# Performance work log

Measured on AMD Instinct MI355X. Metric: run time of the kernel, lower is better.

## Reference

```python
import jax, jax.numpy as jnp
import numpy as np
from jax import lax

BS, C, S = 2, 32, 64  # cubic volume: h == w == d required by the module's views
EPS = 1e-5


def setup_inputs() -> dict:
    key = jax.random.key(0)
    kq, kk, kv, kw, kb, kg = jax.random.split(key, 6)
    q = jax.random.normal(kq, (BS, C, S, S, S), dtype=jnp.float32)
    k = jax.random.normal(kk, (BS, C, S, S, S), dtype=jnp.float32)
    v = jax.random.normal(kv, (BS, C, S, S, S), dtype=jnp.float32)
    # Conv_3x3x3: Conv3d(3*C -> C, k=3, pad=1, bias) + BatchNorm3d(C) (eval) + ReLU
    fan_in = 3 * C * 27
    conv_w = jax.random.normal(kw, (C, 3 * C, 3, 3, 3), dtype=jnp.float32) / np.sqrt(fan_in)
    conv_b = jax.random.normal(kb, (C,), dtype=jnp.float32) * 0.01
    bn_gamma = jnp.ones((C,), jnp.float32)
    bn_beta = jnp.zeros((C,), jnp.float32)
    bn_mean = jnp.zeros((C,), jnp.float32)
    bn_var = jnp.ones((C,), jnp.float32)
    return {"q": q, "k": k, "v": v, "conv_w": conv_w, "conv_b": conv_b,
            "bn_gamma": bn_gamma, "bn_beta": bn_beta, "bn_mean": bn_mean, "bn_var": bn_var}


def _axial_attention(q, k, v):
    # q,k,v: (b, c, h, w, d) with h == w == d == S. All three per-slice python
    # loops of the original collapse into batched einsums (dropout is eval -> identity).
    # Branch a: per d-slice s, A[i,j] = softmax_j(sum_m q[b,c,m,i,s] k[b,c,m,j,s])
    A = jax.nn.softmax(jnp.einsum('bcmis,bcmjs->bcsij', q, k), axis=-1)
    AVa = jnp.einsum('bcsij,bcjws->bciws', A, v)          # (b,c,h,w,d)
    # Branch b: per w-slice s, attention over h with feature dim d
    A = jax.nn.softmax(jnp.einsum('bcism,bcjsm->bcsij', q, k), axis=-1)
    AVb = jnp.einsum('bcsij,bcjsm->bcism', A, v)          # (b,c,h,w,d)
    # Branch c: per h-slice s, attention over w with feature dim d
    A = jax.nn.softmax(jnp.einsum('bcsim,bcsjm->bcsij', q, k), axis=-1)
    AVc = jnp.einsum('bcsij,bcsjm->bcsim', A, v)          # (b,c,h,w,d)
    return jnp.concatenate([AVa, AVb, AVc], axis=1)       # (b,3c,h,w,d)


def reference(q, k, v, conv_w, conv_b, bn_gamma, bn_beta, bn_mean, bn_var):
    x = _axial_attention(q, k, v)
    x = lax.conv_general_dilated(x, conv_w, window_strides=(1, 1, 1), padding='SAME',
                                 dimension_numbers=('NCDHW', 'OIDHW', 'NCDHW'))
    x = x + conv_b[None, :, None, None, None]
    inv = bn_gamma / jnp.sqrt(bn_var + EPS)
    x = x * inv[None, :, None, None, None] + (bn_beta - bn_mean * inv)[None, :, None, None, None]
    return jax.nn.relu(x)
```

## Files before the change

kernel.cpp:

```cpp
#include <hip/hip_runtime.h>
#include <hip/hip_bf16.h>


#define CH 32

typedef __attribute__((ext_vector_type(8))) _Float16 f16x8;
typedef __attribute__((ext_vector_type(4))) _Float16 f16x4;
typedef __attribute__((ext_vector_type(8))) short bf16x8;
typedef __attribute__((ext_vector_type(4))) float f32x4;

static __device__ __forceinline__ unsigned short f2bf(float f) {
  union { float f; unsigned u; } x; x.f = f;
  unsigned r = x.u + 0x7fff + ((x.u >> 16) & 1);
  return (unsigned short)(r >> 16);
}

__global__ __launch_bounds__(256) void trans_dwh(const float* __restrict__ q,
                                                 const float* __restrict__ k,
                                                 const float* __restrict__ v,
                                                 _Float16* __restrict__ qT,
                                                 _Float16* __restrict__ kT,
                                                 _Float16* __restrict__ vT,
                                                 _Float16* __restrict__ qF,
                                                 _Float16* __restrict__ kF,
                                                 _Float16* __restrict__ vF,
                                                 int b) {
  __shared__ __align__(16) _Float16 Ls[64 * 72];
  const int blk = blockIdx.x;
  const int c = blk >> 6;
  const int w = blk & 63;
  const int tid = threadIdx.x;
  const size_t bc = (size_t)(b * CH + c);
  const float* srcs[3] = {q, k, v};
  _Float16* dsts[3] = {qT, kT, vT};
  _Float16* dstsF[3] = {qF, kF, vF};
  const int h = tid >> 2, dq = tid & 3;

  for (int tz = 0; tz < 3; ++tz) {
    const float* sp = srcs[tz] + bc * 262144 + (size_t)h * 4096 + (size_t)w * 64;
    float4 ld[4];
    #pragma unroll
    for (int pp = 0; pp < 4; ++pp) {
      const int d0 = dq * 16 + pp * 4;
      ld[pp] = *(const float4*)(sp + d0);
      Ls[(d0 + 0) * 72 + h] = (_Float16)ld[pp].x;
      Ls[(d0 + 1) * 72 + h] = (_Float16)ld[pp].y;
      Ls[(d0 + 2) * 72 + h] = (_Float16)ld[pp].z;
      Ls[(d0 + 3) * 72 + h] = (_Float16)ld[pp].w;
    }
    {
      _Float16* fp = dstsF[tz] + (size_t)c * 262144 + (size_t)h * 4096 +
                     (size_t)w * 64 + dq * 16;
      f16x8 lo8 = {(_Float16)ld[0].x, (_Float16)ld[0].y, (_Float16)ld[0].z, (_Float16)ld[0].w,
                   (_Float16)ld[1].x, (_Float16)ld[1].y, (_Float16)ld[1].z, (_Float16)ld[1].w};
      f16x8 hi8 = {(_Float16)ld[2].x, (_Float16)ld[2].y, (_Float16)ld[2].z, (_Float16)ld[2].w,
                   (_Float16)ld[3].x, (_Float16)ld[3].y, (_Float16)ld[3].z, (_Float16)ld[3].w};
      *(f16x8*)(fp) = lo8;
      *(f16x8*)(fp + 8) = hi8;
    }
    __syncthreads();
    _Float16* dp = dsts[tz] + (size_t)c * 262144 + (size_t)w * 64;
    #pragma unroll
    for (int p = 0; p < 2; ++p) {
      const int idx = p * 256 + tid;
      const int d = idx >> 3, o = (idx & 7) * 8;
      *(f16x8*)(dp + (size_t)d * 4096 + o) = *(const f16x8*)&Ls[d * 72 + o];
    }
    __syncthreads();
  }
}

__device__ __forceinline__ void attn_core(_Float16 (&Qh)[64][72],
                                          _Float16 (&Kh)[64][72],
                                          _Float16 (&Vh)[64][72],
                                          bool v_transposed,
                                          unsigned short* __restrict__ ydst,
                                          int c, int s, int tid) {
  const int w = tid >> 6;
  const int lane = tid & 63;
  const int r = lane & 15;
  const int oct = lane >> 4;

  f32x4 sc[4];
  #pragma unroll
  for (int jt = 0; jt < 4; ++jt) sc[jt] = (f32x4){0.f, 0.f, 0.f, 0.f};
  f16x8 aq0 = *(const f16x8*)&Qh[w * 16 + r][oct * 8];
  f16x8 aq1 = *(const f16x8*)&Qh[w * 16 + r][32 + oct * 8];
  #pragma unroll
  for (int jt = 0; jt < 4; ++jt) {
    f16x8 bk0 = *(const f16x8*)&Kh[jt * 16 + r][oct * 8];
    f16x8 bk1 = *(const f16x8*)&Kh[jt * 16 + r][32 + oct * 8];
    sc[jt] = __builtin_amdgcn_mfma_f32_16x16x32_f16(aq0, bk0, sc[jt], 0, 0, 0);
    sc[jt] = __builtin_amdgcn_mfma_f32_16x16x32_f16(aq1, bk1, sc[jt], 0, 0, 0);
  }

  float P[4][4];
  #pragma unroll
  for (int reg = 0; reg < 4; ++reg) {
    float mx = fmaxf(fmaxf(sc[0][reg], sc[1][reg]), fmaxf(sc[2][reg], sc[3][reg]));
    mx = fmaxf(mx, __shfl_xor(mx, 1));
    mx = fmaxf(mx, __shfl_xor(mx, 2));
    mx = fmaxf(mx, __shfl_xor(mx, 4));
    mx = fmaxf(mx, __shfl_xor(mx, 8));
    float e[4], sum = 0.f;
    #pragma unroll
    for (int jt = 0; jt < 4; ++jt) { e[jt] = __expf(sc[jt][reg] - mx); sum += e[jt]; }
    sum += __shfl_xor(sum, 1);
    sum += __shfl_xor(sum, 2);
    sum += __shfl_xor(sum, 4);
    sum += __shfl_xor(sum, 8);
    const float inv = 1.f / sum;
    #pragma unroll
    for (int jt = 0; jt < 4; ++jt) P[reg][jt] = e[jt] * inv;
  }

  #pragma unroll
  for (int reg = 0; reg < 4; ++reg)
    #pragma unroll
    for (int jt = 0; jt < 4; ++jt)
      Qh[w * 16 + oct * 4 + reg][jt * 16 + r] = (_Float16)P[reg][jt];

  f16x8 ap0 = *(const f16x8*)&Qh[w * 16 + r][oct * 8];
  f16x8 ap1 = *(const f16x8*)&Qh[w * 16 + r][32 + oct * 8];
  f32x4 ot[4];
  #pragma unroll
  for (int tt = 0; tt < 4; ++tt) {
    ot[tt] = (f32x4){0.f, 0.f, 0.f, 0.f};
    f16x8 bv0, bv1;
    if (v_transposed) {
      bv0 = *(const f16x8*)&Vh[tt * 16 + r][oct * 8];
      bv1 = *(const f16x8*)&Vh[tt * 16 + r][32 + oct * 8];
    } else {
      #pragma unroll
      for (int e = 0; e < 8; ++e) {
        bv0[e] = Vh[oct * 8 + e][tt * 16 + r];
        bv1[e] = Vh[32 + oct * 8 + e][tt * 16 + r];
      }
    }
    ot[tt] = __builtin_amdgcn_mfma_f32_16x16x32_f16(ap0, bv0, ot[tt], 0, 0, 0);
    ot[tt] = __builtin_amdgcn_mfma_f32_16x16x32_f16(ap1, bv1, ot[tt], 0, 0, 0);
  }

  __syncthreads();
  unsigned short* Ot = (unsigned short*)&Kh[0][0];
  #pragma unroll
  for (int tt = 0; tt < 4; ++tt)
    #pragma unroll
    for (int reg = 0; reg < 4; ++reg)
      Ot[(size_t)(w * 16 + oct * 4 + reg) * 72 + tt * 16 + r] = f2bf(ot[tt][reg]);
  __syncthreads();

  {
    const int i = tid >> 2, seg = tid & 3;
    const unsigned short* src = Ot + (size_t)i * 72 + seg * 16;
    bf16x8 a0 = *(const bf16x8*)(src);
    bf16x8 a1 = *(const bf16x8*)(src + 8);
    unsigned short* dst = ydst + ((size_t)(c * 64 + s)) * 4096 + tid * 16;
    *(bf16x8*)(dst) = a0;
    *(bf16x8*)(dst + 8) = a1;
  }
}

__global__ __launch_bounds__(256) void attn0(const _Float16* __restrict__ qT,
                                             const _Float16* __restrict__ kT,
                                             const _Float16* __restrict__ vT,
                                             unsigned short* __restrict__ y0b) {
  __shared__ __align__(16) _Float16 Qh[64][72];
  __shared__ __align__(16) _Float16 Kh[64][72];
  __shared__ __align__(16) _Float16 Vh[64][72];

  const int blk0 = blockIdx.x;
  const int blk = ((blk0 & 7) << 8) | (blk0 >> 3);
  const int s = blk & 63;
  const int c = blk >> 6;
  const int tid = threadIdx.x;

  const _Float16* qp = qT + ((size_t)c * 64 + s) * 4096;
  const _Float16* kp = kT + ((size_t)c * 64 + s) * 4096;
  const _Float16* vp = vT + ((size_t)c * 64 + s) * 4096;
  #pragma unroll
  for (int ii = 0; ii < 2; ++ii) {
    const int idx = ii * 256 + tid;
    const int row = idx >> 3, ch = (idx & 7) * 8;
    *(f16x8*)&Qh[row][ch] = *(const f16x8*)(qp + row * 64 + ch);
    *(f16x8*)&Kh[row][ch] = *(const f16x8*)(kp + row * 64 + ch);
    *(f16x8*)&Vh[row][ch] = *(const f16x8*)(vp + row * 64 + ch);
  }
  __syncthreads();
  attn_core(Qh, Kh, Vh, true, y0b, c, s, tid);
}

__global__ __launch_bounds__(256) void attn12(const _Float16* __restrict__ qF,
                                              const _Float16* __restrict__ kF,
                                              const _Float16* __restrict__ vF,
                                              unsigned short* __restrict__ y1b,
                                              unsigned short* __restrict__ y2b) {
  __shared__ __align__(16) _Float16 Qh[64][72];
  __shared__ __align__(16) _Float16 Kh[64][72];
  __shared__ __align__(16) _Float16 Vh[64][72];

  const int blk0 = blockIdx.x;
  const int blk = ((blk0 & 7) << 9) | (blk0 >> 3);
  const int br2 = blk >> 11;
  const int inner = blk & 2047;
  const int s = inner & 63;
  const int c = inner >> 6;
  const int tid = threadIdx.x;

  const size_t base = (size_t)c * 262144;
  #pragma unroll
  for (int ii = 0; ii < 2; ++ii) {
    const int idx = ii * 256 + tid;
    const int row = idx >> 3, ch = (idx & 7) * 8;
    const size_t off = br2 ? ((size_t)s * 4096 + (size_t)row * 64 + ch)
                           : ((size_t)row * 4096 + (size_t)s * 64 + ch);
    *(f16x8*)&Qh[row][ch] = *(const f16x8*)(qF + base + off);
    *(f16x8*)&Kh[row][ch] = *(const f16x8*)(kF + base + off);
    *(f16x8*)&Vh[row][ch] = *(const f16x8*)(vF + base + off);
  }
  __syncthreads();
  attn_core(Qh, Kh, Vh, false, br2 ? y2b : y1b, c, s, tid);
}

__global__ __launch_bounds__(256) void repack_all(const unsigned short* __restrict__ y0p,
                                                  const unsigned short* __restrict__ y1p,
                                                  const unsigned short* __restrict__ y2p,
                                                  unsigned short* __restrict__ xblk,
                                                  int b) {
  __shared__ unsigned short Ls[32 * 530];
  const int blk = blockIdx.x;
  const int br = blk >> 9;
  const int inner = blk & 511;
  const int oc = inner & 7;
  const int z = inner >> 3;
  const int tid = threadIdx.x;
  const int c = tid & 31;
  const int w8 = tid >> 5;

  const unsigned short* ybr = (br == 0) ? y0p : (br == 1) ? y1p : y2p;

  size_t src;
  if (br == 2) src = ((size_t)(c * 64 + z)) * 4096 + (size_t)(oc * 8 + w8) * 64;
  else         src = ((size_t)(c * 64 + oc * 8 + w8)) * 4096 + (size_t)z * 64;

  #pragma unroll
  for (int kk = 0; kk < 8; ++kk) {
    bf16x8 vv = *(const bf16x8*)(ybr + src + kk * 8);
    #pragma unroll
    for (int e = 0; e < 8; ++e) {
      const int l = kk * 8 + e;
      const int li = (br == 0) ? (l * 8 + w8) : (w8 * 64 + l);
      Ls[c * 530 + li] = (unsigned short)vv[e];
    }
  }
  __syncthreads();

  unsigned short* xq = xblk + ((size_t)(b * 3 + br)) * 262144 * 32;
  #pragma unroll
  for (int p = 0; p < 2; ++p) {
    const int o = p * 256 + tid;
    bf16x8 o0, o1, o2, o3;
    #pragma unroll
    for (int e = 0; e < 8; ++e) {
      o0[e] = (short)Ls[(e)      * 530 + o];
      o1[e] = (short)Ls[(8 + e)  * 530 + o];
      o2[e] = (short)Ls[(16 + e) * 530 + o];
      o3[e] = (short)Ls[(24 + e) * 530 + o];
    }
    int sp;
    if (br == 0) sp = z * 4096 + (o >> 3) * 64 + oc * 8 + (o & 7);
    else         sp = z * 4096 + oc * 512 + o;
    unsigned short* dst = xq + (size_t)sp * 32;
    *(bf16x8*)(dst)      = o0;
    *(bf16x8*)(dst + 8)  = o1;
    *(bf16x8*)(dst + 16) = o2;
    *(bf16x8*)(dst + 24) = o3;
  }
}

__global__ __launch_bounds__(256) void wprep(const float* __restrict__ w,
                                             unsigned short* __restrict__ wt2) {
  int idx = blockIdx.x * 256 + threadIdx.x;
  if (idx >= 27 * 32 * 96) return;
  int tap = idx / 3072;
  int rem = idx - tap * 3072;
  int co = rem / 96, ci = rem - co * 96;
  int ciq = ci >> 5, oct = (ci >> 3) & 3, e = ci & 7;
  wt2[(((tap * 3 + ciq) * 4 + oct) * 32 + co) * 8 + e] =
      f2bf(w[((size_t)co * 96 + ci) * 27 + tap]);
}

__global__ __launch_bounds__(256, 2) void conv_mfma(const unsigned short* __restrict__ xblk,
                                                    const unsigned short* __restrict__ wt2,
                                                    const float* __restrict__ cb,
                                                    const float* __restrict__ gamma,
                                                    const float* __restrict__ beta,
                                                    const float* __restrict__ mean,
                                                    const float* __restrict__ var,
                                                    float* __restrict__ out) {
  __shared__ __align__(16) unsigned short XT[23760];

  const int blk0 = blockIdx.x;
  const int blk = ((blk0 & 7) << 6) | (blk0 >> 3);
  const int yt = blk & 7;
  const int zp = (blk >> 3) & 31;
  const int b = blk >> 8;
  const int tid = threadIdx.x;
  const int w = tid >> 6;
  const int lane = tid & 63;
  const int r = lane & 15;
  const int oct = lane >> 4;
  const int y0 = yt * 8;
  const int z0 = zp * 2;

  f32x4 acc0[2][4][2], acc1[2][4][2];
  #pragma unroll
  for (int ry = 0; ry < 2; ++ry)
    #pragma unroll
    for (int xc = 0; xc < 4; ++xc)
      #pragma unroll
      for (int ct = 0; ct < 2; ++ct) {
        acc0[ry][xc][ct] = (f32x4){0.f, 0.f, 0.f, 0.f};
        acc1[ry][xc][ct] = (f32x4){0.f, 0.f, 0.f, 0.f};
      }

  auto STAGE = [&](int p, int ciq) {
    const unsigned short* xq = xblk + ((size_t)(b * 3 + ciq)) * (262144ull * 32) +
                               (size_t)p * (4096 * 32);
    #pragma unroll
    for (int ii = 0; ii < 11; ++ii) {
      const int idx = ii * 256 + tid;
      if (idx < 2640) {
        const int row = idx / 264;
        const int rem = idx - row * 264;
        const int x = rem >> 2;
        const int cq = rem & 3;
        const int gy = y0 + row - 1, gx = x - 1;
        bf16x8 val = {0, 0, 0, 0, 0, 0, 0, 0};
        if ((unsigned)gy < 64u && (unsigned)gx < 64u)
          val = *(const bf16x8*)(xq + (size_t)(gy * 64 + gx) * 32 + cq * 8);
        *(bf16x8*)&XT[row * 2376 + x * 36 + cq * 8] = val;
      }
    }
  };

  auto C2 = [&](int dzA, int dzB, int ciq) {
    #pragma unroll
    for (int dy = 0; dy < 3; ++dy) {
      #pragma unroll
      for (int dx = 0; dx < 3; ++dx) {
        const unsigned short* wpA =
            wt2 + ((size_t)((((dzA * 3 + dy) * 3 + dx) * 3 + ciq) * 4 + oct)) * 256;
        const unsigned short* wpB =
            wt2 + ((size_t)((((dzB * 3 + dy) * 3 + dx) * 3 + ciq) * 4 + oct)) * 256;
        bf16x8 wA0 = *(const bf16x8*)(wpA + r * 8);
        bf16x8 wA1 = *(const bf16x8*)(wpA + 128 + r * 8);
        bf16x8 wB0 = *(const bf16x8*)(wpB + r * 8);
        bf16x8 wB1 = *(const bf16x8*)(wpB + 128 + r * 8);
        #pragma unroll
        for (int ry = 0; ry < 2; ++ry) {
          const int lrow = w * 2 + ry + dy;
          #pragma unroll
          for (int xc = 0; xc < 4; ++xc) {
            bf16x8 af = *(const bf16x8*)&XT[lrow * 2376 + (xc * 16 + r + dx) * 36 + oct * 8];
            acc0[ry][xc][0] = __builtin_amdgcn_mfma_f32_16x16x32_bf16(af, wA0, acc0[ry][xc][0], 0, 0, 0);
            acc0[ry][xc][1] = __builtin_amdgcn_mfma_f32_16x16x32_bf16(af, wA1, acc0[ry][xc][1], 0, 0, 0);
            acc1[ry][xc][0] = __builtin_amdgcn_mfma_f32_16x16x32_bf16(af, wB0, acc1[ry][xc][0], 0, 0, 0);
            acc1[ry][xc][1] = __builtin_amdgcn_mfma_f32_16x16x32_bf16(af, wB1, acc1[ry][xc][1], 0, 0, 0);
          }
        }
      }
    }
  };

  auto C1 = [&](f32x4 (&A)[2][4][2], int dz, int ciq) {
    #pragma unroll
    for (int dy = 0; dy < 3; ++dy) {
      #pragma unroll
      for (int dx = 0; dx < 3; ++dx) {
        const unsigned short* wp =
            wt2 + ((size_t)((((dz * 3 + dy) * 3 + dx) * 3 + ciq) * 4 + oct)) * 256;
        bf16x8 w0 = *(const bf16x8*)(wp + r * 8);
        bf16x8 w1 = *(const bf16x8*)(wp + 128 + r * 8);
        #pragma unroll
        for (int ry = 0; ry < 2; ++ry) {
          const int lrow = w * 2 + ry + dy;
          #pragma unroll
          for (int xc = 0; xc < 4; ++xc) {
            bf16x8 af = *(const bf16x8*)&XT[lrow * 2376 + (xc * 16 + r + dx) * 36 + oct * 8];
            A[ry][xc][0] = __builtin_amdgcn_mfma_f32_16x16x32_bf16(af, w0, A[ry][xc][0], 0, 0, 0);
            A[ry][xc][1] = __builtin_amdgcn_mfma_f32_16x16x32_bf16(af, w1, A[ry][xc][1], 0, 0, 0);
          }
        }
      }
    }
  };

  #pragma unroll
  for (int ps = 0; ps < 4; ++ps) {
    const int p = z0 - 1 + ps;
    if ((unsigned)p > 63u) continue;
    for (int ciq = 0; ciq < 3; ++ciq) {
      __syncthreads();
      STAGE(p, ciq);
      __syncthreads();
      if (ps == 0)      C1(acc0, 0, ciq);
      else if (ps == 3) C1(acc1, 2, ciq);
      else              C2(ps, ps - 1, ciq);
    }
  }

  float invc[2], shc[2], bic[2];
  #pragma unroll
  for (int ct = 0; ct < 2; ++ct) {
    const int co = ct * 16 + r;
    const float iv = gamma[co] * rsqrtf(var[co] + 1e-5f);
    invc[ct] = iv;
    shc[ct] = beta[co] - mean[co] * iv;
    bic[ct] = cb[co];
  }

  auto STO = [&](f32x4 (&A)[2][4][2], int z) {
    #pragma unroll
    for (int ct = 0; ct < 2; ++ct) {
      float* oc = out + (((size_t)(b * CH + ct * 16 + r)) << 18) + ((size_t)z << 12);
      #pragma unroll
      for (int ry = 0; ry < 2; ++ry) {
        const int y = y0 + w * 2 + ry;
        #pragma unroll
        for (int xc = 0; xc < 4; ++xc) {
          const f32x4 a = A[ry][xc][ct];
          float4 st;
          st.x = fmaxf(0.f, (a[0] + bic[ct]) * invc[ct] + shc[ct]);
          st.y = fmaxf(0.f, (a[1] + bic[ct]) * invc[ct] + shc[ct]);
          st.z = fmaxf(0.f, (a[2] + bic[ct]) * invc[ct] + shc[ct]);
          st.w = fmaxf(0.f, (a[3] + bic[ct]) * invc[ct] + shc[ct]);
          *(float4*)(oc + (size_t)y * 64 + xc * 16 + oct * 4) = st;
        }
      }
    }
  };
  STO(acc0, z0);
  STO(acc1, z0 + 1);
}

extern "C" void kernel_launch(void* const* d_in, const int* in_sizes, int n_in,
                              void* d_out, int out_size, void* d_ws, size_t ws_size,
                              hipStream_t stream) {
  const float* q     = (const float*)d_in[0];
  const float* k     = (const float*)d_in[1];
  const float* v     = (const float*)d_in[2];
  const float* cw    = (const float*)d_in[3];
  const float* cb    = (const float*)d_in[4];
  const float* gamma = (const float*)d_in[5];
  const float* beta  = (const float*)d_in[6];
  const float* mean  = (const float*)d_in[7];
  const float* var   = (const float*)d_in[8];

  unsigned short* xblk = (unsigned short*)d_ws;
  unsigned short* y0b  = (unsigned short*)((char*)d_ws + (96ull  << 20));
  _Float16*       qT   = (_Float16*)((char*)d_ws + (112ull << 20));
  _Float16*       kT   = (_Float16*)((char*)d_ws + (128ull << 20));
  _Float16*       vT   = (_Float16*)((char*)d_ws + (144ull << 20));
  unsigned short* wt2  = (unsigned short*)((char*)d_ws + (160ull << 20));
  _Float16* qF = (_Float16*)((char*)d_ws + (48ull << 20));
  _Float16* kF = (_Float16*)((char*)d_ws + (64ull << 20));
  _Float16* vF = (_Float16*)((char*)d_ws + (80ull << 20));
  unsigned short* y1b = (unsigned short*)kT;
  unsigned short* y2b = (unsigned short*)vT;
  float* out = (float*)d_out;

  hipLaunchKernelGGL(wprep, dim3(324), dim3(256), 0, stream, cw, wt2);
  for (int b = 0; b < 2; ++b) {
    hipLaunchKernelGGL(trans_dwh, dim3(2048), dim3(256), 0, stream,
                       q, k, v, qT, kT, vT, qF, kF, vF, b);
    hipLaunchKernelGGL(attn0, dim3(2048), dim3(256), 0, stream, qT, kT, vT, y0b);
    hipLaunchKernelGGL(attn12, dim3(4096), dim3(256), 0, stream,
                       qF, kF, vF, y1b, y2b);
    hipLaunchKernelGGL(repack_all, dim3(1536), dim3(256), 0, stream,
                       y0b, y1b, y2b, xblk, b);
  }
  hipLaunchKernelGGL(conv_mfma, dim3(512), dim3(256), 0, stream,
                     xblk, wt2, cb, gamma, beta, mean, var, out);
}
```

Before: 333.5 us.

## Switch conv to 32x32x16 bf16 MFMA with weights as A operand

The 3D conv kernel moves from 16x16x32 MFMA tiles to 32x32x16 tiles, with the weights as the A operand (32 output channels) and 32 x-positions as B. The weight prep is re-laid out per lane to match the new operand format. Each tile now reuses more operands per instruction, so fewer LDS reads and weight loads are issued per FLOP. The cost is that the epilogue now writes scalar floats per channel register rather than float4 vectors, and per-channel BN constants are recomputed inside the store loop.

```diff
diff --git a/kernel.cpp b/kernel.cpp
--- a/kernel.cpp
+++ b/kernel.cpp
@@ -8,6 +8,7 @@
 typedef __attribute__((ext_vector_type(4))) _Float16 f16x4;
 typedef __attribute__((ext_vector_type(8))) short bf16x8;
 typedef __attribute__((ext_vector_type(4))) float f32x4;
+typedef __attribute__((ext_vector_type(16))) float f32x16;
 
 static __device__ __forceinline__ unsigned short f2bf(float f) {
   union { float f; unsigned u; } x; x.f = f;
@@ -279,19 +280,20 @@
 }
 
 __global__ __launch_bounds__(256) void wprep(const float* __restrict__ w,
-                                             unsigned short* __restrict__ wt2) {
+                                             unsigned short* __restrict__ wt3) {
   int idx = blockIdx.x * 256 + threadIdx.x;
-  if (idx >= 27 * 32 * 96) return;
-  int tap = idx / 3072;
-  int rem = idx - tap * 3072;
-  int co = rem / 96, ci = rem - co * 96;
-  int ciq = ci >> 5, oct = (ci >> 3) & 3, e = ci & 7;
-  wt2[(((tap * 3 + ciq) * 4 + oct) * 32 + co) * 8 + e] =
-      f2bf(w[((size_t)co * 96 + ci) * 27 + tap]);
+  if (idx >= 27 * 6 * 64 * 8) return;
+  const int e = idx & 7;
+  const int lane = (idx >> 3) & 63;
+  const int rest = idx >> 9;
+  const int tap = rest / 6, ksg = rest - tap * 6;
+  const int co = lane & 31, kg = lane >> 5;
+  const int ci = ksg * 16 + kg * 8 + e;
+  wt3[idx] = f2bf(w[((size_t)co * 96 + ci) * 27 + tap]);
 }
 
 __global__ __launch_bounds__(256, 2) void conv_mfma(const unsigned short* __restrict__ xblk,
-                                                    const unsigned short* __restrict__ wt2,
+                                                    const unsigned short* __restrict__ wt3,
                                                     const float* __restrict__ cb,
                                                     const float* __restrict__ gamma,
                                                     const float* __restrict__ beta,
@@ -308,20 +310,20 @@
   const int tid = threadIdx.x;
   const int w = tid >> 6;
   const int lane = tid & 63;
-  const int r = lane & 15;
-  const int oct = lane >> 4;
+  const int x32 = lane & 31;
+  const int kg = lane >> 5;
   const int y0 = yt * 8;
   const int z0 = zp * 2;
 
-  f32x4 acc0[2][4][2], acc1[2][4][2];
+  f32x16 acc0[2][2], acc1[2][2];
   #pragma unroll
   for (int ry = 0; ry < 2; ++ry)
     #pragma unroll
-    for (int xc = 0; xc < 4; ++xc)
+    for (int xc = 0; xc < 2; ++xc)
       #pragma unroll
-      for (int ct = 0; ct < 2; ++ct) {
-        acc0[ry][xc][ct] = (f32x4){0.f, 0.f, 0.f, 0.f};
-        acc1[ry][xc][ct] = (f32x4){0.f, 0.f, 0.f, 0.f};
+      for (int e = 0; e < 16; ++e) {
+        acc0[ry][xc][e] = 0.f;
+        acc1[ry][xc][e] = 0.f;
       }
 
   auto STAGE = [&](int p, int ciq) {
@@ -346,50 +348,52 @@
 
   auto C2 = [&](int dzA, int dzB, int ciq) {
     #pragma unroll
-    for (int dy = 0; dy < 3; ++dy) {
+    for (int ks = 0; ks < 2; ++ks) {
       #pragma unroll
-      for (int dx = 0; dx < 3; ++dx) {
-        const unsigned short* wpA =
-            wt2 + ((size_t)((((dzA * 3 + dy) * 3 + dx) * 3 + ciq) * 4 + oct)) * 256;
-        const unsigned short* wpB =
-            wt2 + ((size_t)((((dzB * 3 + dy) * 3 + dx) * 3 + ciq) * 4 + oct)) * 256;
-        bf16x8 wA0 = *(const bf16x8*)(wpA + r * 8);
-        bf16x8 wA1 = *(const bf16x8*)(wpA + 128 + r * 8);
-        bf16x8 wB0 = *(const bf16x8*)(wpB + r * 8);
-        bf16x8 wB1 = *(const bf16x8*)(wpB + 128 + r * 8);
+      for (int dy = 0; dy < 3; ++dy) {
         #pragma unroll
-        for (int ry = 0; ry < 2; ++ry) {
-          const int lrow = w * 2 + ry + dy;
+        for (int dx = 0; dx < 3; ++dx) {
+          const unsigned short* wpA =
+              wt3 + ((size_t)(((dzA * 3 + dy) * 3 + dx) * 6 + ciq * 2 + ks) * 64 + lane) * 8;
+          const unsigned short* wpB =
+              wt3 + ((size_t)(((dzB * 3 + dy) * 3 + dx) * 6 + ciq * 2 + ks) * 64 + lane) * 8;
+          bf16x8 wA = *(const bf16x8*)wpA;
+          bf16x8 wB = *(const bf16x8*)wpB;
           #pragma unroll
-          for (int xc = 0; xc < 4; ++xc) {
-            bf16x8 af = *(const bf16x8*)&XT[lrow * 2376 + (xc * 16 + r + dx) * 36 + oct * 8];
-            acc0[ry][xc][0] = __builtin_amdgcn_mfma_f32_16x16x32_bf16(af, wA0, acc0[ry][xc][0], 0, 0, 0);
-            acc0[ry][xc][1] = __builtin_amdgcn_mfma_f32_16x16x32_bf16(af, wA1, acc0[ry][xc][1], 0, 0, 0);
-            acc1[ry][xc][0] = __builtin_amdgcn_mfma_f32_16x16x32_bf16(af, wB0, acc1[ry][xc][0], 0, 0, 0);
-            acc1[ry][xc][1] = __builtin_amdgcn_mfma_f32_16x16x32_bf16(af, wB1, acc1[ry][xc][1], 0, 0, 0);
+          for (int ry = 0; ry < 2; ++ry) {
+            const int lrow = w * 2 + ry + dy;
+            #pragma unroll
+            for (int xc = 0; xc < 2; ++xc) {
+              bf16x8 af = *(const bf16x8*)&XT[lrow * 2376 + (xc * 32 + x32 + dx) * 36 +
+                                              (ks * 2 + kg) * 8];
+              acc0[ry][xc] = __builtin_amdgcn_mfma_f32_32x32x16_bf16(wA, af, acc0[ry][xc], 0, 0, 0);
+              acc1[ry][xc] = __builtin_amdgcn_mfma_f32_32x32x16_bf16(wB, af, acc1[ry][xc], 0, 0, 0);
+            }
           }
         }
       }
     }
   };
 
-  auto C1 = [&](f32x4 (&A)[2][4][2], int dz, int ciq) {
-    #pragma unroll
-    for (int dy = 0; dy < 3; ++dy) {
+  auto C1 = [&](f32x16 (&A)[2][2], int dz, int ciq) {
+    #pragma unroll
+    for (int ks = 0; ks < 2; ++ks) {
       #pragma unroll
-      for (int dx = 0; dx < 3; ++dx) {
-        const unsigned short* wp =
-            wt2 + ((size_t)((((dz * 3 + dy) * 3 + dx) * 3 + ciq) * 4 + oct)) * 256;
-        bf16x8 w0 = *(const bf16x8*)(wp + r * 8);
-        bf16x8 w1 = *(const bf16x8*)(wp + 128 + r * 8);
+      for (int dy = 0; dy < 3; ++dy) {
         #pragma unroll
-        for (int ry = 0; ry < 2; ++ry) {
-          const int lrow = w * 2 + ry + dy;
+        for (int dx = 0; dx < 3; ++dx) {
+          const unsigned short* wp =
+              wt3 + ((size_t)(((dz * 3 + dy) * 3 + dx) * 6 + ciq * 2 + ks) * 64 + lane) * 8;
+          bf16x8 wf = *(const bf16x8*)wp;
           #pragma unroll
-          for (int xc = 0; xc < 4; ++xc) {
-            bf16x8 af = *(const bf16x8*)&XT[lrow * 2376 + (xc * 16 + r + dx) * 36 + oct * 8];
-            A[ry][xc][0] = __builtin_amdgcn_mfma_f32_16x16x32_bf16(af, w0, A[ry][xc][0], 0, 0, 0);
-            A[ry][xc][1] = __builtin_amdgcn_mfma_f32_16x16x32_bf16(af, w1, A[ry][xc][1], 0, 0, 0);
+          for (int ry = 0; ry < 2; ++ry) {
+            const int lrow = w * 2 + ry + dy;
+            #pragma unroll
+            for (int xc = 0; xc < 2; ++xc) {
+              bf16x8 af = *(const bf16x8*)&XT[lrow * 2376 + (xc * 32 + x32 + dx) * 36 +
+                                              (ks * 2 + kg) * 8];
+              A[ry][xc] = __builtin_amdgcn_mfma_f32_32x32x16_bf16(wf, af, A[ry][xc], 0, 0, 0);
+            }
           }
         }
       }
@@ -410,32 +414,19 @@
     }
   }
 
-  float invc[2], shc[2], bic[2];
-  #pragma unroll
-  for (int ct = 0; ct < 2; ++ct) {
-    const int co = ct * 16 + r;
-    const float iv = gamma[co] * rsqrtf(var[co] + 1e-5f);
-    invc[ct] = iv;
-    shc[ct] = beta[co] - mean[co] * iv;
-    bic[ct] = cb[co];
-  }
-
-  auto STO = [&](f32x4 (&A)[2][4][2], int z) {
-    #pragma unroll
-    for (int ct = 0; ct < 2; ++ct) {
-      float* oc = out + (((size_t)(b * CH + ct * 16 + r)) << 18) + ((size_t)z << 12);
+  auto STO = [&](f32x16 (&A)[2][2], int z) {
+    #pragma unroll
+    for (int reg = 0; reg < 16; ++reg) {
+      const int co = (reg & 3) + 8 * (reg >> 2) + 4 * kg;
+      const float iv = gamma[co] * rsqrtf(var[co] + 1e-5f);
+      const float of = beta[co] - mean[co] * iv + cb[co] * iv;
+      float* oc = out + (((size_t)(b * CH + co)) << 18) + ((size_t)z << 12);
       #pragma unroll
       for (int ry = 0; ry < 2; ++ry) {
         const int y = y0 + w * 2 + ry;
         #pragma unroll
-        for (int xc = 0; xc < 4; ++xc) {
-          const f32x4 a = A[ry][xc][ct];
-          float4 st;
-          st.x = fmaxf(0.f, (a[0] + bic[ct]) * invc[ct] + shc[ct]);
-          st.y = fmaxf(0.f, (a[1] + bic[ct]) * invc[ct] + shc[ct]);
-          st.z = fmaxf(0.f, (a[2] + bic[ct]) * invc[ct] + shc[ct]);
-          st.w = fmaxf(0.f, (a[3] + bic[ct]) * invc[ct] + shc[ct]);
-          *(float4*)(oc + (size_t)y * 64 + xc * 16 + oct * 4) = st;
+        for (int xc = 0; xc < 2; ++xc) {
+          oc[(size_t)y * 64 + xc * 32 + x32] = fmaxf(0.f, A[ry][xc][reg] * iv + of);
         }
       }
     }
@@ -462,7 +453,7 @@
   _Float16*       qT   = (_Float16*)((char*)d_ws + (112ull << 20));
   _Float16*       kT   = (_Float16*)((char*)d_ws + (128ull << 20));
   _Float16*       vT   = (_Float16*)((char*)d_ws + (144ull << 20));
-  unsigned short* wt2  = (unsigned short*)((char*)d_ws + (160ull << 20));
+  unsigned short* wt3  = (unsigned short*)((char*)d_ws + (160ull << 20));
   _Float16* qF = (_Float16*)((char*)d_ws + (48ull << 20));
   _Float16* kF = (_Float16*)((char*)d_ws + (64ull << 20));
   _Float16* vF = (_Float16*)((char*)d_ws + (80ull << 20));
@@ -470,7 +461,7 @@
   unsigned short* y2b = (unsigned short*)vT;
   float* out = (float*)d_out;
 
-  hipLaunchKernelGGL(wprep, dim3(324), dim3(256), 0, stream, cw, wt2);
+  hipLaunchKernelGGL(wprep, dim3(324), dim3(256), 0, stream, cw, wt3);
   for (int b = 0; b < 2; ++b) {
     hipLaunchKernelGGL(trans_dwh, dim3(2048), dim3(256), 0, stream,
                        q, k, v, qT, kT, vT, qF, kF, vF, b);
@@ -481,5 +472,5 @@
                        y0b, y1b, y2b, xblk, b);
   }
   hipLaunchKernelGGL(conv_mfma, dim3(512), dim3(256), 0, stream,
-                     xblk, wt2, cb, gamma, beta, mean, var, out);
-}
+                     xblk, wt3, cb, gamma, beta, mean, var, out);
+}
```

Result: slower. 359.3 us (+7.7%).
